# Kernel optimization log

Measured on AMD Instinct MI355X. Metric: run time of the kernel, lower is better.

Reference implementation:

```python
import jax, jax.numpy as jnp
import numpy as np

B, S, D, H = 2, 2048, 1024, 16
HD = D // H  # 64

def setup_inputs() -> dict:
    key = jax.random.key(0)
    ks = jax.random.split(key, 6)
    s = 1.0 / np.sqrt(D)
    return {
        "x": jax.random.normal(ks[0], (B, S, D), dtype=jnp.float32),
        "wq": jax.random.normal(ks[1], (D, D), dtype=jnp.float32) * s,
        "wk": jax.random.normal(ks[2], (D, D), dtype=jnp.float32) * s,
        "wv": jax.random.normal(ks[3], (D, D), dtype=jnp.float32) * s,
        "wo": jax.random.normal(ks[4], (D, D), dtype=jnp.float32) * s,
        "bo": jax.random.normal(ks[5], (D,), dtype=jnp.float32) * 0.01,
    }

def reference(x, wq, wk, wv, wo, bo):
    b, s, _ = x.shape
    # QKV projections (qkvBias=False), reshape to [b, h, s, hd]
    q = (x @ wq).reshape(b, s, H, HD).transpose(0, 2, 1, 3)
    k = (x @ wk).reshape(b, s, H, HD).transpose(0, 2, 1, 3)
    v = (x @ wv).reshape(b, s, H, HD).transpose(0, 2, 1, 3)
    # scores, causal mask (upper triangle -> -inf), scale, softmax
    scores = jnp.einsum('bhqd,bhkd->bhqk', q, k)
    causal = jnp.triu(jnp.ones((s, s), dtype=bool), k=1)
    scores = jnp.where(causal, -jnp.inf, scores) / np.sqrt(HD)
    weights = jax.nn.softmax(scores, axis=-1)  # dropout=0 (eval)
    ctx = jnp.einsum('bhqk,bhkd->bhqd', weights, v)
    ctx = ctx.transpose(0, 2, 1, 3).reshape(b, s, D)
    return ctx @ wo + bo
```

## Files before the change

### kernel.cpp

```cpp
#include <hip/hip_runtime.h>
#include <hip/hip_bf16.h>
#include <math.h>

#define BB 2
#define SS 2048
#define DD 1024
#define HH 16
#define HDIM 64

typedef unsigned short u16;
typedef __attribute__((ext_vector_type(8))) short bfrag;
typedef __attribute__((ext_vector_type(4))) short s16x4;
typedef __attribute__((ext_vector_type(4))) float f32x4;

#define NEG_BIG (-1e30f)
#define QSCALE 0.18033688011112042f

__device__ __forceinline__ u16 f2u(float f) {
    unsigned int u = __builtin_bit_cast(unsigned int, f);
    u += 0x7fffu + ((u >> 16) & 1u);
    return (u16)(u >> 16);
}

__device__ __forceinline__ float fexp2(float x) {
#if __has_builtin(__builtin_amdgcn_exp2f)
    return __builtin_amdgcn_exp2f(x);
#else
    return exp2f(x);
#endif
}

__device__ __forceinline__ void async16(const u16* g, u16* l) {
    __builtin_amdgcn_global_load_lds((__attribute__((address_space(1))) void*)g,
                                     (__attribute__((address_space(3))) void*)l,
                                     16, 0, 0);
}

__device__ __forceinline__ f32x4 mfma16(bfrag a, bfrag b, f32x4 c) {
    return __builtin_amdgcn_mfma_f32_16x16x32_bf16(a, b, c, 0, 0, 0);
}

__device__ __forceinline__ f32x4 mfma_pv(s16x4 a, s16x4 b, f32x4 c) {
#if __has_builtin(__builtin_amdgcn_mfma_f32_16x16x16_bf16)
    return __builtin_amdgcn_mfma_f32_16x16x16_bf16(a, b, c, 0, 0, 0);
#elif __has_builtin(__builtin_amdgcn_mfma_f32_16x16x16bf16_1k)
    return __builtin_amdgcn_mfma_f32_16x16x16bf16_1k(a, b, c, 0, 0, 0);
#else
    f32x4 d;
    asm("v_mfma_f32_16x16x16_bf16 %0, %1, %2, %3" : "=v"(d) : "v"(a), "v"(b), "v"(c));
    return d;
#endif
}

__global__ __launch_bounds__(256) void prep_k(
    const float* __restrict__ x,  u16* __restrict__ xb,
    const float* __restrict__ wq, const float* __restrict__ wk,
    const float* __restrict__ wv, const float* __restrict__ wo,
    u16* __restrict__ wT)
{
    const int id = blockIdx.x;
    const int t = threadIdx.x;
    if (id < 2048) {
        int i = (id * 256 + t) * 8;
        float4 a = *(const float4*)(x + i);
        float4 b = *(const float4*)(x + i + 4);
        u16 o[8] = { f2u(a.x), f2u(a.y), f2u(a.z), f2u(a.w),
                     f2u(b.x), f2u(b.y), f2u(b.z), f2u(b.w) };
        *(uint4*)(xb + i) = *(uint4*)o;
        return;
    }
    const int wid = id - 2048;
    const int z = wid >> 8;
    const int kt = wid & 15, nt = (wid >> 4) & 15;
    const float* w = (z == 0) ? wq : (z == 1) ? wk : (z == 2) ? wv : wo;
    u16* o = wT + (size_t)z * DD * DD;
    __shared__ __align__(16) u16 T[64][72];
    const int k0 = kt * 64, n0 = nt * 64;
    {
        int kr = t >> 2, nb = (t & 3) * 16;
        const float4* s4 = (const float4*)(w + (size_t)(k0 + kr) * DD + n0 + nb);
        #pragma unroll
        for (int jj = 0; jj < 4; ++jj) {
            float4 v = s4[jj];
            T[kr][nb + jj*4 + 0] = f2u(v.x);
            T[kr][nb + jj*4 + 1] = f2u(v.y);
            T[kr][nb + jj*4 + 2] = f2u(v.z);
            T[kr][nb + jj*4 + 3] = f2u(v.w);
        }
    }
    __syncthreads();
    {
        int nr = t >> 2, kb = (t & 3) * 16;
        u16 tmp[16];
        #pragma unroll
        for (int j = 0; j < 16; ++j) tmp[j] = T[kb + j][nr];
        *(uint4*)(o + (size_t)(n0 + nr) * DD + k0 + kb)     = ((uint4*)tmp)[0];
        *(uint4*)(o + (size_t)(n0 + nr) * DD + k0 + kb + 8) = ((uint4*)tmp)[1];
    }
}

__global__ __launch_bounds__(256) void gemm_qkv_k(
    const u16* __restrict__ xb, const u16* __restrict__ wT,
    u16* __restrict__ Qo, u16* __restrict__ Ko, u16* __restrict__ Vt)
{
    const u16* wTz = wT + (size_t)blockIdx.z * DD * DD;
    const float osc = (blockIdx.z == 0) ? QSCALE : 1.0f;

    __shared__ __align__(16) u16 As[128 * 64];
    __shared__ __align__(16) u16 Bs[64 * 64];

    const int t = threadIdx.x;
    const int m0 = blockIdx.x * 128, n0 = blockIdx.y * 64;
    const int lane15 = t & 15, quad = (t >> 4) & 3, wave = t >> 6;
    const int wm = wave & 1, wn = wave >> 1;

    int arow[4], acol[4];
    #pragma unroll
    for (int i = 0; i < 4; ++i) {
        int c = t + i * 256;
        arow[i] = c >> 3;
        acol[i] = (c & 7) ^ (arow[i] & 7);
    }
    const int br0 = t >> 3,         bs0 = t & 7;
    const int br1 = (t + 256) >> 3, bs1 = (t + 256) & 7;
    const int bc0 = bs0 ^ (br0 & 7);
    const int bc1 = bs1 ^ (br1 & 7);
    const int ldb = (t & 192) * 8;

    int aoff[4][2], boff[2][2];
    #pragma unroll
    for (int mi = 0; mi < 4; ++mi) {
        int r = wm * 64 + mi * 16 + lane15;
        #pragma unroll
        for (int kh = 0; kh < 2; ++kh)
            aoff[mi][kh] = (r * 8 + ((kh * 4 + quad) ^ (r & 7))) * 8;
    }
    #pragma unroll
    for (int ni = 0; ni < 2; ++ni) {
        int r = wn * 32 + ni * 16 + lane15;
        #pragma unroll
        for (int kh = 0; kh < 2; ++kh)
            boff[ni][kh] = (r * 8 + ((kh * 4 + quad) ^ (r & 7))) * 8;
    }

    f32x4 acc[4][2];
    #pragma unroll
    for (int mi = 0; mi < 4; ++mi)
        #pragma unroll
        for (int ni = 0; ni < 2; ++ni)
            acc[mi][ni] = (f32x4){0.f, 0.f, 0.f, 0.f};

    for (int it = 0; it < 16; ++it) {
        const int k0 = it * 64;
        #pragma unroll
        for (int i = 0; i < 4; ++i)
            async16(xb + (size_t)(m0 + arow[i]) * DD + k0 + acol[i] * 8,
                    As + ldb + i * 2048);
        async16(wTz + (size_t)(n0 + br0) * DD + k0 + bc0 * 8, Bs + ldb);
        async16(wTz + (size_t)(n0 + br1) * DD + k0 + bc1 * 8, Bs + ldb + 2048);
        __syncthreads();
        #pragma unroll
        for (int kh = 0; kh < 2; ++kh) {
            bfrag av[4], bv[2];
            #pragma unroll
            for (int mi = 0; mi < 4; ++mi) av[mi] = *(const bfrag*)(As + aoff[mi][kh]);
            #pragma unroll
            for (int ni = 0; ni < 2; ++ni) bv[ni] = *(const bfrag*)(Bs + boff[ni][kh]);
            #pragma unroll
            for (int mi = 0; mi < 4; ++mi)
                #pragma unroll
                for (int ni = 0; ni < 2; ++ni)
                    acc[mi][ni] = mfma16(av[mi], bv[ni], acc[mi][ni]);
        }
        __syncthreads();
    }

    const int h = n0 >> 6;
    const int bq = m0 >> 11;
    const int ms = m0 & (SS - 1);

    if (blockIdx.z != 2) {
        u16* out = (blockIdx.z == 0) ? Qo : Ko;
        u16* dst = out + (((size_t)(bq * HH + h)) * SS) * HDIM;
        #pragma unroll
        for (int mi = 0; mi < 4; ++mi) {
            #pragma unroll
            for (int r = 0; r < 4; ++r) {
                int s = ms + wm * 64 + mi * 16 + quad * 4 + r;
                #pragma unroll
                for (int ni = 0; ni < 2; ++ni) {
                    int hd = wn * 32 + ni * 16 + lane15;
                    dst[(size_t)s * HDIM + hd] = f2u(acc[mi][ni][r] * osc);
                }
            }
        }
    } else {
        u16* T = As;
        __syncthreads();
        #pragma unroll
        for (int mi = 0; mi < 4; ++mi)
            #pragma unroll
            for (int r = 0; r < 4; ++r) {
                int ml = wm * 64 + mi * 16 + quad * 4 + r;
                #pragma unroll
                for (int ni = 0; ni < 2; ++ni) {
                    int nl = wn * 32 + ni * 16 + lane15;
                    T[nl * 128 + (ml ^ ((nl & 7) << 4))] = f2u(acc[mi][ni][r]);
                }
            }
        __syncthreads();
        u16* dst = Vt + ((size_t)(bq * HH + h)) * (HDIM * SS);
        #pragma unroll
        for (int i = 0; i < 4; ++i) {
            int c = t + i * 256;
            int row = c >> 4;
            int mb  = (c & 15) * 8;
            uint4 val = *(const uint4*)&T[row * 128 + (mb ^ ((row & 7) << 4))];
            *(uint4*)(dst + (size_t)row * SS + ms + mb) = val;
        }
    }
}

__global__ __launch_bounds__(256) void gemm_out_k(
    const u16* __restrict__ ctxb, const u16* __restrict__ woT,
    const float* __restrict__ bo, float* __restrict__ out)
{
    __shared__ __align__(16) u16 As[2][4096];
    __shared__ __align__(16) u16 Bs[2][4096];

    const int t = threadIdx.x;
    const int m0 = blockIdx.x * 64, n0 = blockIdx.y * 64;
    const int lane15 = t & 15, quad = (t >> 4) & 3, wave = t >> 6;
    const int wm = wave & 1, wn = wave >> 1;

    const int br0 = t >> 3,         bs0 = t & 7;
    const int br1 = (t + 256) >> 3, bs1 = (t + 256) & 7;
    const int bc0 = bs0 ^ (br0 & 7);
    const int bc1 = bs1 ^ (br1 & 7);
    const int ldb = (t & 192) * 8;

    int aoff[2][2], boff[2][2];
    #pragma unroll
    for (int mi = 0; mi < 2; ++mi) {
        int r = wm * 32 + mi * 16 + lane15;
        #pragma unroll
        for (int kh = 0; kh < 2; ++kh)
            aoff[mi][kh] = (r * 8 + ((kh * 4 + quad) ^ (r & 7))) * 8;
    }
    #pragma unroll
    for (int ni = 0; ni < 2; ++ni) {
        int r = wn * 32 + ni * 16 + lane15;
        #pragma unroll
        for (int kh = 0; kh < 2; ++kh)
            boff[ni][kh] = (r * 8 + ((kh * 4 + quad) ^ (r & 7))) * 8;
    }

    f32x4 acc[2][2];
    #pragma unroll
    for (int mi = 0; mi < 2; ++mi)
        #pragma unroll
        for (int ni = 0; ni < 2; ++ni)
            acc[mi][ni] = (f32x4){0.f, 0.f, 0.f, 0.f};

    for (int it = 0; it < 8; ++it) {
        const int k0 = it * 128;
        #pragma unroll
        for (int hh = 0; hh < 2; ++hh) {
            const int kh64 = k0 + hh * 64;
            async16(ctxb + (size_t)(m0 + br0) * DD + kh64 + bc0 * 8, &As[hh][ldb]);
            async16(ctxb + (size_t)(m0 + br1) * DD + kh64 + bc1 * 8, &As[hh][ldb + 2048]);
            async16(woT  + (size_t)(n0 + br0) * DD + kh64 + bc0 * 8, &Bs[hh][ldb]);
            async16(woT  + (size_t)(n0 + br1) * DD + kh64 + bc1 * 8, &Bs[hh][ldb + 2048]);
        }
        __syncthreads();
        #pragma unroll
        for (int hh = 0; hh < 2; ++hh) {
            #pragma unroll
            for (int kh = 0; kh < 2; ++kh) {
                bfrag av[2], bv[2];
                #pragma unroll
                for (int mi = 0; mi < 2; ++mi) av[mi] = *(const bfrag*)&As[hh][aoff[mi][kh]];
                #pragma unroll
                for (int ni = 0; ni < 2; ++ni) bv[ni] = *(const bfrag*)&Bs[hh][boff[ni][kh]];
                #pragma unroll
                for (int mi = 0; mi < 2; ++mi)
                    #pragma unroll
                    for (int ni = 0; ni < 2; ++ni)
                        acc[mi][ni] = mfma16(av[mi], bv[ni], acc[mi][ni]);
            }
        }
        __syncthreads();
    }

    float bias[2];
    #pragma unroll
    for (int ni = 0; ni < 2; ++ni)
        bias[ni] = bo[n0 + wn * 32 + ni * 16 + lane15];

    #pragma unroll
    for (int mi = 0; mi < 2; ++mi) {
        #pragma unroll
        for (int r = 0; r < 4; ++r) {
            int m = m0 + wm * 32 + mi * 16 + quad * 4 + r;
            #pragma unroll
            for (int ni = 0; ni < 2; ++ni) {
                int n = n0 + wn * 32 + ni * 16 + lane15;
                out[(size_t)m * DD + n] = acc[mi][ni][r] + bias[ni];
            }
        }
    }
}

template<bool MASKED>
__device__ __forceinline__ void qkt_pv(
    const u16* __restrict__ Kc, const u16* __restrict__ Vc,
    const bfrag bq[2], const int koff[2], const int voff[4],
    int kv0, int qg, int quad4, f32x4 acc_o[4], f32x4& acc_s, s16x4 ones4)
{
    f32x4 sT[4];
    #pragma unroll
    for (int ni = 0; ni < 4; ++ni) sT[ni] = (f32x4){0.f, 0.f, 0.f, 0.f};

    __builtin_amdgcn_s_setprio(1);
    #pragma unroll
    for (int kh = 0; kh < 2; ++kh)
        #pragma unroll
        for (int ni = 0; ni < 4; ++ni)
            sT[ni] = mfma16(*(const bfrag*)&Kc[koff[kh] + ni * 1024], bq[kh], sT[ni]);
    __builtin_amdgcn_s_setprio(0);

    #pragma unroll
    for (int ni = 0; ni < 4; ++ni) {
        float pv[4];
        #pragma unroll
        for (int r = 0; r < 4; ++r) {
            float v = sT[ni][r];
            if (MASKED) {
                int kvg = kv0 + ni * 16 + quad4 + r;
                if (kvg > qg) v = NEG_BIG;
            }
            pv[r] = fexp2(v);
        }
        unsigned lo = __builtin_amdgcn_perm(
            __builtin_bit_cast(unsigned, pv[1]),
            __builtin_bit_cast(unsigned, pv[0]), 0x07060302u);
        unsigned hi = __builtin_amdgcn_perm(
            __builtin_bit_cast(unsigned, pv[3]),
            __builtin_bit_cast(unsigned, pv[2]), 0x07060302u);
        s16x4 pf = __builtin_bit_cast(s16x4,
            ((unsigned long long)hi << 32) | (unsigned long long)lo);
        __builtin_amdgcn_s_setprio(1);
        acc_s = mfma_pv(ones4, pf, acc_s);
        #pragma unroll
        for (int nd = 0; nd < 4; ++nd)
            acc_o[nd] = mfma_pv(*(const s16x4*)&Vc[voff[ni] + nd * 1024],
                                pf, acc_o[nd]);
        __builtin_amdgcn_s_setprio(0);
    }
}

__global__ __launch_bounds__(256, 5) void attn_k(
    const u16* __restrict__ Q, const u16* __restrict__ K,
    const u16* __restrict__ Vt, u16* __restrict__ ctx)
{
    __shared__ __align__(16) u16 Ks[2][64 * 64];
    __shared__ __align__(16) u16 Vs[2][64 * 64];
    const int t = threadIdx.x;
    const int lane15 = t & 15, quad = (t >> 4) & 3, wave = t >> 6;
    const int bh = blockIdx.x;
    const int yy = (int)blockIdx.y;
    const int y0 = yy & 7, rnd = yy >> 3;
    const int qt = (rnd == 0) ? 31 - y0 : (rnd == 1) ? y0
                 : (rnd == 2) ? 23 - y0 : 8 + y0;
    const int q0 = qt * 64;
    const int b = bh >> 4, h = bh & 15;
    const u16* Qb = Q  + (size_t)bh * SS * HDIM;
    const u16* Kb = K  + (size_t)bh * SS * HDIM;
    const u16* Vb = Vt + (size_t)bh * HDIM * SS;

    const int kr0 = t >> 3,         ks0 = t & 7;
    const int kr1 = (t + 256) >> 3, ks1 = (t + 256) & 7;
    const int kc0 = ks0 ^ (kr0 & 7);
    const int kc1 = ks1 ^ (kr1 & 7);
    const int ldst = (t & 192) * 8;

    const u16* kga = Kb + (size_t)kr0 * HDIM + kc0 * 8;
    const u16* kgb = Kb + (size_t)kr1 * HDIM + kc1 * 8;
    const u16* vga = Vb + (size_t)kr0 * SS + kc0 * 8;
    const u16* vgb = Vb + (size_t)kr1 * SS + kc1 * 8;

    async16(Qb + (size_t)(q0 + kr0) * HDIM + kc0 * 8, &Ks[1][ldst]);
    async16(Qb + (size_t)(q0 + kr1) * HDIM + kc1 * 8, &Ks[1][ldst + 2048]);
    async16(kga, &Ks[0][ldst]);
    async16(kgb, &Ks[0][ldst + 2048]);
    async16(vga, &Vs[0][ldst]);
    async16(vgb, &Vs[0][ldst + 2048]);

    const int r7 = lane15 & 7;
    int koff[2];
    #pragma unroll
    for (int kh = 0; kh < 2; ++kh)
        koff[kh] = (lane15 * 8 + ((kh * 4 + quad) ^ r7)) * 8;
    int voff[4];
    #pragma unroll
    for (int ni = 0; ni < 4; ++ni)
        voff[ni] = (lane15 * 8 + ((ni * 2 + (quad >> 1)) ^ r7)) * 8 + (quad & 1) * 4;

    __syncthreads();
    bfrag bq[2];
    bq[0] = *(const bfrag*)&Ks[1][koff[0] + wave * 1024];
    bq[1] = *(const bfrag*)&Ks[1][koff[1] + wave * 1024];
    __syncthreads();

    s16x4 ones4;
    #pragma unroll
    for (int i = 0; i < 4; ++i) ones4[i] = (short)0x3f80;

    f32x4 acc_o[4];
    f32x4 acc_s = (f32x4){0.f, 0.f, 0.f, 0.f};
    #pragma unroll
    for (int nd = 0; nd < 4; ++nd) acc_o[nd] = (f32x4){0.f, 0.f, 0.f, 0.f};

    const int qg = q0 + wave * 16 + lane15;
    const int quad4 = quad * 4;

    const u16* kpa = kga + 64 * HDIM;
    const u16* kpb = kgb + 64 * HDIM;
    const u16* vpa = vga + 64;
    const u16* vpb = vgb + 64;

    for (int kt = 0; kt < qt; ++kt) {
        const int pb = (kt + 1) & 1;
        async16(kpa, &Ks[pb][ldst]);
        async16(kpb, &Ks[pb][ldst + 2048]);
        async16(vpa, &Vs[pb][ldst]);
        async16(vpb, &Vs[pb][ldst + 2048]);
        kpa += 64 * HDIM; kpb += 64 * HDIM;
        vpa += 64;        vpb += 64;
        qkt_pv<false>(Ks[kt & 1], Vs[kt & 1], bq, koff, voff,
                      kt * 64, qg, quad4, acc_o, acc_s, ones4);
        __syncthreads();
    }
    qkt_pv<true>(Ks[qt & 1], Vs[qt & 1], bq, koff, voff,
                 qt * 64, qg, quad4, acc_o, acc_s, ones4);

    const float inv = 1.f / acc_s[0];
    const int srow = q0 + wave * 16 + lane15;
    u16* dst = ctx + ((size_t)b * SS + srow) * DD + h * HDIM + quad4;
    #pragma unroll
    for (int nd = 0; nd < 4; ++nd) {
        uint2 stw;
        stw.x = (unsigned)f2u(acc_o[nd][0] * inv) |
                ((unsigned)f2u(acc_o[nd][1] * inv) << 16);
        stw.y = (unsigned)f2u(acc_o[nd][2] * inv) |
                ((unsigned)f2u(acc_o[nd][3] * inv) << 16);
        *(uint2*)(dst + nd * 16) = stw;
    }
}

extern "C" void kernel_launch(void* const* d_in, const int* in_sizes, int n_in,
                              void* d_out, int out_size, void* d_ws, size_t ws_size,
                              hipStream_t stream) {
    const float* x  = (const float*)d_in[0];
    const float* wq = (const float*)d_in[1];
    const float* wk = (const float*)d_in[2];
    const float* wv = (const float*)d_in[3];
    const float* wo = (const float*)d_in[4];
    const float* bo = (const float*)d_in[5];
    float* out = (float*)d_out;

    char* ws = (char*)d_ws;
    const size_t MB8 = (size_t)8 * 1024 * 1024;
    u16* xb  = (u16*)(ws);
    u16* wT  = (u16*)(ws + MB8);
    u16* Qb  = (u16*)(ws + 2 * MB8);
    u16* Kb  = (u16*)(ws + 3 * MB8);
    u16* Vt  = (u16*)(ws + 4 * MB8);
    u16* ctxb = xb;

    prep_k    <<<3072, 256, 0, stream>>>(x, xb, wq, wk, wv, wo, wT);
    gemm_qkv_k<<<dim3(32, 16, 3), 256, 0, stream>>>(xb, wT, Qb, Kb, Vt);
    attn_k    <<<dim3(32, 32), 256, 0, stream>>>(Qb, Kb, Vt, ctxb);
    gemm_out_k<<<dim3(64, 16), 256, 0, stream>>>(ctxb, wT + (size_t)3 * DD * DD, bo, out);
}
```

Baseline: 169.6 us.

## Triple-buffer K/V tiles with one barrier per step and direct Q register loads

The attention kernel moves from double to triple-buffered LDS for K/V tiles and prefetches two tiles ahead. A partial vmcnt wait plus a single barrier per iteration replaces the trailing __syncthreads. Q fragments now load straight from global memory into registers instead of going through LDS with two barriers. LDS use rises and launch bounds drop from 5 to 3 blocks per SM, which may reduce occupancy. It also relies on vmcnt counting of the async loads being exact.

```diff
diff --git a/kernel.cpp b/kernel.cpp
--- a/kernel.cpp
+++ b/kernel.cpp
@@ -359,12 +359,12 @@
     }
 }
 
-__global__ __launch_bounds__(256, 5) void attn_k(
+__global__ __launch_bounds__(256, 3) void attn_k(
     const u16* __restrict__ Q, const u16* __restrict__ K,
     const u16* __restrict__ Vt, u16* __restrict__ ctx)
 {
-    __shared__ __align__(16) u16 Ks[2][64 * 64];
-    __shared__ __align__(16) u16 Vs[2][64 * 64];
+    __shared__ __align__(16) u16 Ks[3][64 * 64];
+    __shared__ __align__(16) u16 Vs[3][64 * 64];
     const int t = threadIdx.x;
     const int lane15 = t & 15, quad = (t >> 4) & 3, wave = t >> 6;
     const int bh = blockIdx.x;
@@ -389,28 +389,36 @@
     const u16* vga = Vb + (size_t)kr0 * SS + kc0 * 8;
     const u16* vgb = Vb + (size_t)kr1 * SS + kc1 * 8;
 
-    async16(Qb + (size_t)(q0 + kr0) * HDIM + kc0 * 8, &Ks[1][ldst]);
-    async16(Qb + (size_t)(q0 + kr1) * HDIM + kc1 * 8, &Ks[1][ldst + 2048]);
+    const int r7 = lane15 & 7;
+    int koff[2];
+    #pragma unroll
+    for (int kh = 0; kh < 2; ++kh)
+        koff[kh] = (lane15 * 8 + ((kh * 4 + quad) ^ r7)) * 8;
+    int voff[4];
+    #pragma unroll
+    for (int ni = 0; ni < 4; ++ni)
+        voff[ni] = (lane15 * 8 + ((ni * 2 + (quad >> 1)) ^ r7)) * 8 + (quad & 1) * 4;
+
+    const int qrow = q0 + wave * 16 + lane15;
+    bfrag bq[2];
+    bq[0] = *(const bfrag*)(Qb + (size_t)qrow * HDIM + quad * 8);
+    bq[1] = *(const bfrag*)(Qb + (size_t)qrow * HDIM + 32 + quad * 8);
+    asm volatile("s_waitcnt vmcnt(0)" ::: "memory");
+
     async16(kga, &Ks[0][ldst]);
     async16(kgb, &Ks[0][ldst + 2048]);
     async16(vga, &Vs[0][ldst]);
     async16(vgb, &Vs[0][ldst + 2048]);
-
-    const int r7 = lane15 & 7;
-    int koff[2];
-    #pragma unroll
-    for (int kh = 0; kh < 2; ++kh)
-        koff[kh] = (lane15 * 8 + ((kh * 4 + quad) ^ r7)) * 8;
-    int voff[4];
-    #pragma unroll
-    for (int ni = 0; ni < 4; ++ni)
-        voff[ni] = (lane15 * 8 + ((ni * 2 + (quad >> 1)) ^ r7)) * 8 + (quad & 1) * 4;
-
-    __syncthreads();
-    bfrag bq[2];
-    bq[0] = *(const bfrag*)&Ks[1][koff[0] + wave * 1024];
-    bq[1] = *(const bfrag*)&Ks[1][koff[1] + wave * 1024];
-    __syncthreads();
+    if (qt >= 1) {
+        async16(kga + 64 * HDIM, &Ks[1][ldst]);
+        async16(kgb + 64 * HDIM, &Ks[1][ldst + 2048]);
+        async16(vga + 64, &Vs[1][ldst]);
+        async16(vgb + 64, &Vs[1][ldst + 2048]);
+    }
+    const u16* kpa = kga + 2 * 64 * HDIM;
+    const u16* kpb = kgb + 2 * 64 * HDIM;
+    const u16* vpa = vga + 2 * 64;
+    const u16* vpb = vgb + 2 * 64;
 
     s16x4 ones4;
     #pragma unroll
@@ -421,32 +429,35 @@
     #pragma unroll
     for (int nd = 0; nd < 4; ++nd) acc_o[nd] = (f32x4){0.f, 0.f, 0.f, 0.f};
 
-    const int qg = q0 + wave * 16 + lane15;
+    const int qg = qrow;
     const int quad4 = quad * 4;
 
-    const u16* kpa = kga + 64 * HDIM;
-    const u16* kpb = kgb + 64 * HDIM;
-    const u16* vpa = vga + 64;
-    const u16* vpb = vgb + 64;
+    int cb = 0;
+    int ib = 2;
 
     for (int kt = 0; kt < qt; ++kt) {
-        const int pb = (kt + 1) & 1;
-        async16(kpa, &Ks[pb][ldst]);
-        async16(kpb, &Ks[pb][ldst + 2048]);
-        async16(vpa, &Vs[pb][ldst]);
-        async16(vpb, &Vs[pb][ldst + 2048]);
-        kpa += 64 * HDIM; kpb += 64 * HDIM;
-        vpa += 64;        vpb += 64;
-        qkt_pv<false>(Ks[kt & 1], Vs[kt & 1], bq, koff, voff,
+        asm volatile("s_waitcnt vmcnt(4)" ::: "memory");
+        __builtin_amdgcn_s_barrier();
+        if (kt + 2 <= qt) {
+            async16(kpa, &Ks[ib][ldst]);
+            async16(kpb, &Ks[ib][ldst + 2048]);
+            async16(vpa, &Vs[ib][ldst]);
+            async16(vpb, &Vs[ib][ldst + 2048]);
+            kpa += 64 * HDIM; kpb += 64 * HDIM;
+            vpa += 64;        vpb += 64;
+            ib = (ib == 2) ? 0 : ib + 1;
+        }
+        qkt_pv<false>(Ks[cb], Vs[cb], bq, koff, voff,
                       kt * 64, qg, quad4, acc_o, acc_s, ones4);
-        __syncthreads();
-    }
-    qkt_pv<true>(Ks[qt & 1], Vs[qt & 1], bq, koff, voff,
+        cb = (cb == 2) ? 0 : cb + 1;
+    }
+    asm volatile("s_waitcnt vmcnt(0)" ::: "memory");
+    __builtin_amdgcn_s_barrier();
+    qkt_pv<true>(Ks[cb], Vs[cb], bq, koff, voff,
                  qt * 64, qg, quad4, acc_o, acc_s, ones4);
 
     const float inv = 1.f / acc_s[0];
-    const int srow = q0 + wave * 16 + lane15;
-    u16* dst = ctx + ((size_t)b * SS + srow) * DD + h * HDIM + quad4;
+    u16* dst = ctx + ((size_t)b * SS + qrow) * DD + h * HDIM + quad4;
     #pragma unroll
     for (int nd = 0; nd < 4; ++nd) {
         uint2 stw;
```

Measured after the change: 171.5 us. Within noise of the previous version (+1.1%).
